# Optimization experiments

Hardware: AMD Instinct MI355X
Metric: run time of the kernel (lower is better)

## Reference

```python
import jax, jax.numpy as jnp
import numpy as np

D_MODEL = 1024
N_HEADS = 16
HEAD_DIM = D_MODEL // N_HEADS
B, T_Q, T_CACHE = 2, 2048, 2048


def setup_inputs() -> dict:
    key = jax.random.key(0)
    ks = jax.random.split(key, 12)
    s = 1.0 / np.sqrt(D_MODEL)
    return {
        "x": jax.random.normal(ks[0], (B, T_Q, D_MODEL), jnp.float32),
        "k_cache": jax.random.normal(ks[1], (B, N_HEADS, T_CACHE, HEAD_DIM), jnp.float32),
        "v_cache": jax.random.normal(ks[2], (B, N_HEADS, T_CACHE, HEAD_DIM), jnp.float32),
        "Wq": jax.random.normal(ks[3], (D_MODEL, D_MODEL), jnp.float32) * s,
        "bq": jax.random.normal(ks[4], (D_MODEL,), jnp.float32) * s,
        "Wk": jax.random.normal(ks[5], (D_MODEL, D_MODEL), jnp.float32) * s,
        "bk": jax.random.normal(ks[6], (D_MODEL,), jnp.float32) * s,
        "Wv": jax.random.normal(ks[7], (D_MODEL, D_MODEL), jnp.float32) * s,
        "bv": jax.random.normal(ks[8], (D_MODEL,), jnp.float32) * s,
        "Wo": jax.random.normal(ks[9], (D_MODEL, D_MODEL), jnp.float32) * s,
        "bo": jax.random.normal(ks[10], (D_MODEL,), jnp.float32) * s,
    }


def reference(x, k_cache, v_cache, Wq, bq, Wk, bk, Wv, bv, Wo, bo):
    B_, T, C = x.shape
    H, Dh = N_HEADS, HEAD_DIM
    scale = Dh ** -0.5

    def proj(W, b):
        # [B,T,C] -> [B,H,T,Dh]
        y = jnp.einsum('btc,cd->btd', x, W) + b
        return y.reshape(B_, T, H, Dh).transpose(0, 2, 1, 3)

    q = proj(Wq, bq)
    k = jnp.concatenate([k_cache, proj(Wk, bk)], axis=2)
    v = jnp.concatenate([v_cache, proj(Wv, bv)], axis=2)

    Tq, Tk = q.shape[2], k.shape[2]
    scores = jnp.einsum('bhqd,bhkd->bhqk', q, k) * scale  # [B,H,Tq,Tk]
    # causal: query i attends to keys j <= i + (Tk - Tq)
    i = jnp.arange(Tq)[:, None]
    j = jnp.arange(Tk)[None, :]
    mask = j > i + (Tk - Tq)
    scores = jnp.where(mask, -jnp.inf, scores)
    attn = jax.nn.softmax(scores, axis=-1)
    out = jnp.einsum('bhqk,bhkd->bhqd', attn, v)
    out = out.transpose(0, 2, 1, 3).reshape(B_, T, C)
    out = jnp.einsum('btc,cd->btd', out, Wo) + bo
    return out, (k, v)
```

## Files before the change

kernel.cpp:

```cpp
#include <hip/hip_runtime.h>
#include <hip/hip_bf16.h>
#include <cstdint>
#include <cstddef>

#define DM 1024
#define NH 16
#define DH 64
#define BB 2
#define TQ 2048
#define TCACHE 2048
#define TKTOT 4096
#define MROWS 4096

typedef __attribute__((ext_vector_type(8))) short bf16x8;
typedef __attribute__((ext_vector_type(4))) short bf16x4;
typedef __attribute__((ext_vector_type(4))) float f32x4;
typedef __attribute__((ext_vector_type(16))) float f32x16;

__device__ __forceinline__ unsigned pk2(float a, float b) {
  unsigned r;
  asm("v_cvt_pk_bf16_f32 %0, %1, %2" : "=v"(r) : "v"(a), "v"(b));
  return r;
}

__device__ __forceinline__ short f2bf(float f) {
  return (short)(unsigned short)pk2(f, f);
}

__device__ __forceinline__ uint2 pk4(float x, float y, float z, float w) {
  uint2 r;
  r.x = pk2(x, y);
  r.y = pk2(z, w);
  return r;
}

__device__ __forceinline__ float bf2f(short s) {
  union { unsigned u; float f; } v;
  v.u = ((unsigned)(unsigned short)s) << 16;
  return v.f;
}

__device__ __forceinline__ float exp2fast(float x) {
#if __has_builtin(__builtin_amdgcn_exp2f)
  return __builtin_amdgcn_exp2f(x);
#else
  return exp2f(x);
#endif
}

__device__ __forceinline__ void plswap(unsigned& a, unsigned& b) {
  asm volatile("v_permlane32_swap_b32 %0, %1" : "+v"(a), "+v"(b));
}

__device__ __forceinline__ void gld_lds16(const short* g, short* l) {
  __builtin_amdgcn_global_load_lds(
      (const __attribute__((address_space(1))) void*)((uintptr_t)g),
      (__attribute__((address_space(3))) void*)((uintptr_t)l), 16, 0, 0);
}

__global__ __launch_bounds__(256) void k_prep(
    const float* __restrict__ x, short* __restrict__ xb,
    const float* __restrict__ W0, const float* __restrict__ W1,
    const float* __restrict__ W2, const float* __restrict__ W3,
    short* __restrict__ Wt,
    const float* __restrict__ kc, short* __restrict__ Kb,
    const float* __restrict__ vc, short* __restrict__ Vtb) {
  __shared__ short lds[64 * 65];
  const int bid = (int)blockIdx.x;
  if (bid < 4096) {
    const size_t i = (size_t)bid * 256 + threadIdx.x;
    const float4 v = ((const float4*)x)[i];
    *(uint2*)(((short4*)xb) + i) = pk4(v.x, v.y, v.z, v.w);
  } else if (bid < 8192) {
    const int local = bid - 4096;
    const int bx = local & 31, by = (local >> 5) & 31, bz = local >> 10;
    short (*tile)[33] = (short(*)[33])lds;
    const float* W = (bz == 0) ? W0 : (bz == 1) ? W1 : (bz == 2) ? W2 : W3;
    short* dst = Wt + (size_t)bz * DM * DM;
    const int k0 = by * 32, n0 = bx * 32;
    const int tx = threadIdx.x & 31, ty = threadIdx.x >> 5;
#pragma unroll
    for (int r = 0; r < 4; r++) {
      const int k = ty + r * 8;
      tile[k][tx] = f2bf(W[(size_t)(k0 + k) * DM + n0 + tx]);
    }
    __syncthreads();
#pragma unroll
    for (int r = 0; r < 4; r++) {
      const int n = ty + r * 8;
      dst[(size_t)(n0 + n) * DM + k0 + tx] = tile[tx][n];
    }
  } else if (bid < 12288) {
    const size_t i = (size_t)(bid - 8192) * 256 + threadIdx.x;
    const float4 v = ((const float4*)kc)[i];
    const size_t e = i * 4;
    const int dh = (int)(e & 63);
    const int t = (int)((e >> 6) & 2047);
    const int bh = (int)(e >> 17);
    *(uint2*)(Kb + ((size_t)bh * TKTOT + t) * DH + dh) = pk4(v.x, v.y, v.z, v.w);
  } else {
    const int local = bid - 12288;
    const int bh = local >> 5;
    const int t0 = (local & 31) * 64;
    short (*tile)[65] = (short(*)[65])lds;
    const int tx = threadIdx.x & 15, ty = threadIdx.x >> 4;
    const float* src = vc + ((size_t)bh * TCACHE + t0) * DH;
#pragma unroll
    for (int r = 0; r < 4; r++) {
      const int t = ty + r * 16;
      const float4 v = *(const float4*)(src + (size_t)t * DH + tx * 4);
      tile[tx * 4 + 0][t] = f2bf(v.x);
      tile[tx * 4 + 1][t] = f2bf(v.y);
      tile[tx * 4 + 2][t] = f2bf(v.z);
      tile[tx * 4 + 3][t] = f2bf(v.w);
    }
    __syncthreads();
    short* vt = Vtb + (size_t)bh * DH * TKTOT + t0;
#pragma unroll
    for (int r = 0; r < 4; r++) {
      const int dh = ty + r * 16;
      short4 o;
      o.x = tile[dh][tx * 4 + 0];
      o.y = tile[dh][tx * 4 + 1];
      o.z = tile[dh][tx * 4 + 2];
      o.w = tile[dh][tx * 4 + 3];
      *(short4*)(vt + (size_t)dh * TKTOT + tx * 4) = o;
    }
  }
}

__global__ __launch_bounds__(256) void k_gemm(
    const short* __restrict__ A, const short* __restrict__ Bt,
    const float* __restrict__ b0, const float* __restrict__ b1, const float* __restrict__ b2,
    const int is_qkv, float* __restrict__ fdst,
    short* __restrict__ Qb, short* __restrict__ Kb, short* __restrict__ Vtb) {
  const int z = is_qkv ? (int)blockIdx.z : 3;
  const short* Bz = Bt + (is_qkv ? (size_t)z * DM * DM : 0);
  const float* bias = (z == 0 || z == 3) ? b0 : (z == 1 ? b1 : b2);

  __shared__ short sA[2][128 * 32];
  __shared__ short sB[2][128 * 32];

  const int m0 = blockIdx.y * 128;
  const int n0 = blockIdx.x * 128;
  const int tid = threadIdx.x;
  const int wv = tid >> 6;
  const int lane = tid & 63;
  const int quad = lane >> 4;
  const int l16 = lane & 15;
  const int wm = (wv >> 1) * 64;
  const int wn = (wv & 1) * 64;

  const f32x4 zero = {0.f, 0.f, 0.f, 0.f};
  f32x4 acc[4][4];
#pragma unroll
  for (int i = 0; i < 4; i++)
#pragma unroll
    for (int j = 0; j < 4; j++) acc[i][j] = zero;

  const int sw = (quad ^ ((l16 >> 1) & 3)) << 4;
  const int afo = (wm + l16) * 64 + sw;
  const int bfo = (wn + l16) * 64 + sw;

#define STAGEG(k0_, b_)                                                         \
  do {                                                                          \
    _Pragma("unroll") for (int s = 0; s < 2; s++) {                             \
      const int c = tid + s * 256;                                              \
      const int row = c >> 2, cs = c & 3;                                       \
      const int gc = cs ^ ((row >> 1) & 3);                                     \
      gld_lds16(A + (size_t)(m0 + row) * DM + (k0_) + gc * 8, &sA[b_][c * 8]);  \
      gld_lds16(Bz + (size_t)(n0 + row) * DM + (k0_) + gc * 8, &sB[b_][c * 8]); \
    }                                                                           \
  } while (0)

  STAGEG(0, 0);
  __syncthreads();
  int buf = 0;
  for (int k0 = 0; k0 < DM; k0 += 32) {
    if (k0 + 32 < DM) STAGEG(k0 + 32, buf ^ 1);
    const char* Ab = (const char*)&sA[0][0] + buf * 8192;
    const char* Bb = (const char*)&sB[0][0] + buf * 8192;
    bf16x8 af[4], bfv[4];
#pragma unroll
    for (int i = 0; i < 4; i++) af[i] = *(const bf16x8*)(Ab + afo + i * 1024);
#pragma unroll
    for (int j = 0; j < 4; j++) bfv[j] = *(const bf16x8*)(Bb + bfo + j * 1024);
    __builtin_amdgcn_s_setprio(1);
#pragma unroll
    for (int i = 0; i < 4; i++)
#pragma unroll
      for (int j = 0; j < 4; j++)
        acc[i][j] = __builtin_amdgcn_mfma_f32_16x16x32_bf16(af[i], bfv[j], acc[i][j], 0, 0, 0);
    __builtin_amdgcn_s_setprio(0);
    __syncthreads();
    buf ^= 1;
  }
#undef STAGEG

#pragma unroll
  for (int i = 0; i < 4; i++) {
#pragma unroll
    for (int j = 0; j < 4; j++) {
      const int gn = n0 + wn + j * 16 + l16;
      const float bb = bias[gn];
#pragma unroll
      for (int r = 0; r < 4; r++) {
        const int gm = m0 + wm + i * 16 + quad * 4 + r;
        const float v = acc[i][j][r] + bb;
        if (z == 3) {
          fdst[(size_t)gm * DM + gn] = v;
        } else {
          const int b_ = gm >> 11, t = gm & 2047;
          const int h_ = gn >> 6, dh = gn & 63;
          if (z == 0) {
            Qb[(((size_t)(b_ * NH + h_)) * TQ + t) * DH + dh] = f2bf(v * 0.18033688011f);
          } else if (z == 1) {
            Kb[(((size_t)(b_ * NH + h_)) * TKTOT + TCACHE + t) * DH + dh] = f2bf(v);
          } else {
            Vtb[(((size_t)(b_ * NH + h_)) * DH + dh) * TKTOT + TCACHE + t] = f2bf(v);
          }
        }
      }
    }
  }
}

__global__ __launch_bounds__(256, 4) void k_attn_expand(
    const short* __restrict__ Qb, const short* __restrict__ Kb,
    const short* __restrict__ Vtb, short* __restrict__ AOb,
    const float* __restrict__ kc, float* __restrict__ kF,
    const float* __restrict__ vc, float* __restrict__ vF) {
  __shared__ short SH[16384];

  const int bid = (int)blockIdx.x;
  if (bid < 512) {
    const int y = bid >> 5;
    const int bh = bid & 31;
    const int qx = (y < 8) ? (15 - y) : (y - 8);
    const int q0 = qx * 128;
    const int tid = threadIdx.x;
    const int wq = tid >> 6;
    const int lane = tid & 63;
    const int l32 = lane & 31;
    const int h = lane >> 5;

    const int nkt = 2 * qx + 34;

    const short* Kg = Kb + (size_t)bh * TKTOT * DH;
    const short* Vtg = Vtb + (size_t)bh * DH * TKTOT;

    const int c0 = tid, c1 = tid + 256;
    const int r0 = c0 >> 3, g0 = ((c0 & 7) ^ (r0 & 7)) * 8;
    const int r1 = c1 >> 3, g1 = ((c1 & 7) ^ (r1 & 7)) * 8;
    const short* Kst0 = Kg + (size_t)r0 * DH + g0;
    const short* Kst1 = Kg + (size_t)r1 * DH + g1;
    const short* Vst0 = Vtg + (size_t)r0 * TKTOT + g0;
    const short* Vst1 = Vtg + (size_t)r1 * TKTOT + g1;

    const short* Qrow = Qb + ((size_t)bh * TQ + q0 + wq * 32 + l32) * DH;
    bf16x8 qf[4];
#pragma unroll
    for (int s = 0; s < 4; s++) qf[s] = *(const bf16x8*)(Qrow + s * 16 + h * 8);

    const char* sKc = (const char*)SH;
    const char* sVc = (const char*)SH + 16384;
    const int rx7 = l32 & 7;
    const int base0 = l32 * 128;
    const int base1 = base0 + 4096;
    int co[4];
#pragma unroll
    for (int ks = 0; ks < 4; ks++) co[ks] = ((2 * ks + h) ^ rx7) << 4;

    const f32x16 zerov = {0, 0, 0, 0, 0, 0, 0, 0, 0, 0, 0, 0, 0, 0, 0, 0};
    f32x16 of0 = zerov;
    f32x16 of1 = zerov;
    float la = 0.f, lb = 0.f, lc = 0.f, ld = 0.f;

#define STAGE(t_, b_)                                    \
    do {                                                 \
      const size_t koff = (size_t)(t_) * 64 * DH;        \
      const size_t voff = (size_t)(t_) * 64;             \
      short* dK = SH + (b_)*4096;                        \
      short* dV = SH + 8192 + (b_)*4096;                 \
      gld_lds16(Kst0 + koff, dK + c0 * 8);               \
      gld_lds16(Kst1 + koff, dK + c1 * 8);               \
      gld_lds16(Vst0 + voff, dV + c0 * 8);               \
      gld_lds16(Vst1 + voff, dV + c1 * 8);               \
    } while (0)

    STAGE(0, 0);
    __syncthreads();
    int buf = 0;

    for (int t = 0; t < nkt; t++) {
      if (t + 1 < nkt) STAGE(t + 1, buf ^ 1);
      const char* kb_ = sKc + buf * 8192;
      const char* vb_ = sVc + buf * 8192;

      f32x16 sacc0, sacc1;
      __builtin_amdgcn_s_setprio(1);
      {
        const bf16x8 kf0 = *(const bf16x8*)(kb_ + base0 + co[0]);
        const bf16x8 kf1 = *(const bf16x8*)(kb_ + base1 + co[0]);
        sacc0 = __builtin_amdgcn_mfma_f32_32x32x16_bf16(kf0, qf[0], zerov, 0, 0, 0);
        sacc1 = __builtin_amdgcn_mfma_f32_32x32x16_bf16(kf1, qf[0], zerov, 0, 0, 0);
      }
#pragma unroll
      for (int ks = 1; ks < 4; ks++) {
        const bf16x8 kf0 = *(const bf16x8*)(kb_ + base0 + co[ks]);
        const bf16x8 kf1 = *(const bf16x8*)(kb_ + base1 + co[ks]);
        sacc0 = __builtin_amdgcn_mfma_f32_32x32x16_bf16(kf0, qf[ks], sacc0, 0, 0, 0);
        sacc1 = __builtin_amdgcn_mfma_f32_32x32x16_bf16(kf1, qf[ks], sacc1, 0, 0, 0);
      }
      __builtin_amdgcn_s_setprio(0);

      if (t >= nkt - 2) {
        const int qgl = q0 + wq * 32 + l32 + TCACHE;
        const int kb0 = t * 64 + 4 * h;
#pragma unroll
        for (int r = 0; r < 16; r++) {
          const int key = kb0 + (r & 3) + 8 * (r >> 2);
          if (key > qgl) sacc0[r] = -1e30f;
          if (key + 32 > qgl) sacc1[r] = -1e30f;
        }
      }
#pragma unroll
      for (int r = 0; r < 16; r++) {
        const float e0 = exp2fast(sacc0[r]);
        const float e1 = exp2fast(sacc1[r]);
        sacc0[r] = e0;
        sacc1[r] = e1;
        if ((r & 3) == 0) la += e0 + e1;
        else if ((r & 3) == 1) lb += e0 + e1;
        else if ((r & 3) == 2) lc += e0 + e1;
        else ld += e0 + e1;
      }

      bf16x8 pa[4];
#pragma unroll
      for (int s = 0; s < 4; s++) {
        const int o = (s & 1) * 8;
        unsigned w0, w1, w2, w3;
        if (s < 2) {
          w0 = pk2(sacc0[o + 0], sacc0[o + 1]);
          w1 = pk2(sacc0[o + 2], sacc0[o + 3]);
          w2 = pk2(sacc0[o + 4], sacc0[o + 5]);
          w3 = pk2(sacc0[o + 6], sacc0[o + 7]);
        } else {
          w0 = pk2(sacc1[o + 0], sacc1[o + 1]);
          w1 = pk2(sacc1[o + 2], sacc1[o + 3]);
          w2 = pk2(sacc1[o + 4], sacc1[o + 5]);
          w3 = pk2(sacc1[o + 6], sacc1[o + 7]);
        }
        plswap(w0, w2);
        plswap(w1, w3);
        union { unsigned u[4]; bf16x8 v; } pu;
        pu.u[0] = w0; pu.u[1] = w1; pu.u[2] = w2; pu.u[3] = w3;
        pa[s] = pu.v;
      }

      __builtin_amdgcn_s_setprio(1);
#pragma unroll
      for (int ks = 0; ks < 4; ks++) {
        const bf16x8 vf0 = *(const bf16x8*)(vb_ + base0 + co[ks]);
        const bf16x8 vf1 = *(const bf16x8*)(vb_ + base1 + co[ks]);
        of0 = __builtin_amdgcn_mfma_f32_32x32x16_bf16(pa[ks], vf0, of0, 0, 0, 0);
        of1 = __builtin_amdgcn_mfma_f32_32x32x16_bf16(pa[ks], vf1, of1, 0, 0, 0);
      }
      __builtin_amdgcn_s_setprio(0);
      __syncthreads();
      buf ^= 1;
    }
#undef STAGE

    float* sLf = (float*)SH;
    const float l_lane = (la + lb) + (lc + ld);
    const float l_tot = l_lane + __shfl_xor(l_lane, 32);
    if (h == 0) sLf[wq * 32 + l32] = l_tot;
    const int b_ = bh >> 4, h_ = bh & 15;
#pragma unroll
    for (int r = 0; r < 16; r++) {
      const int row = (r & 3) + 8 * (r >> 2) + 4 * h;
      const float inv = 1.f / sLf[wq * 32 + row];
      const int qg = q0 + wq * 32 + row;
      short* d = AOb + ((size_t)(b_ * TQ + qg)) * DM + h_ * 64;
      d[l32] = f2bf(of0[r] * inv);
      d[32 + l32] = f2bf(of1[r] * inv);
    }
  } else if (bid < 8704) {
    const size_t f4 = (size_t)(bid - 512) * 256 + threadIdx.x;
    const size_t e = f4 * 4;
    const int t = (int)((e >> 6) & 4095);
    float4 v;
    if (t < TCACHE) {
      const int dh = (int)(e & 63);
      const int bh = (int)(e >> 18);
      v = *(const float4*)(kc + ((size_t)(bh * TCACHE + t)) * DH + dh);
    } else {
      const short4 s = *(const short4*)(Kb + e);
      v.x = bf2f(s.x); v.y = bf2f(s.y); v.z = bf2f(s.z); v.w = bf2f(s.w);
    }
    *(float4*)(kF + e) = v;
  } else {
    const int local = bid - 8704;
    const int tt = local & 63, bh = local >> 6;
    short* tile = SH;
    if (tt < 32) {
#pragma unroll
      for (int k2 = 0; k2 < 4; k2++) {
        const int f = threadIdx.x + k2 * 256;
        const int trow = f >> 4, dh4 = f & 15;
        const size_t si = ((size_t)(bh * TCACHE) + tt * 64 + trow) * DH + dh4 * 4;
        const size_t di = ((size_t)(bh * TKTOT) + tt * 64 + trow) * DH + dh4 * 4;
        *(float4*)(vF + di) = *(const float4*)(vc + si);
      }
    } else {
      const int t0 = tt * 64;
#pragma unroll
      for (int k2 = 0; k2 < 4; k2++) {
        const int f = threadIdx.x + k2 * 256;
        const int dh = f >> 4, tc4 = f & 15;
        const short4 s = *(const short4*)(Vtb + ((size_t)(bh * DH + dh)) * TKTOT + t0 + tc4 * 4);
        *(short4*)(&tile[dh * 72 + tc4 * 4]) = s;
      }
      __syncthreads();
#pragma unroll
      for (int k2 = 0; k2 < 4; k2++) {
        const int f = threadIdx.x + k2 * 256;
        const int trow = f >> 4, dh4 = f & 15;
        float4 v;
        v.x = bf2f(tile[(dh4 * 4 + 0) * 72 + trow]);
        v.y = bf2f(tile[(dh4 * 4 + 1) * 72 + trow]);
        v.z = bf2f(tile[(dh4 * 4 + 2) * 72 + trow]);
        v.w = bf2f(tile[(dh4 * 4 + 3) * 72 + trow]);
        *(float4*)(vF + ((size_t)(bh * TKTOT) + t0 + trow) * DH + dh4 * 4) = v;
      }
    }
  }
}


extern "C" void kernel_launch(void* const* d_in, const int* in_sizes, int n_in,
                              void* d_out, int out_size, void* d_ws, size_t ws_size,
                              hipStream_t stream) {
  const float* x = (const float*)d_in[0];
  const float* kc = (const float*)d_in[1];
  const float* vc = (const float*)d_in[2];
  const float* Wq = (const float*)d_in[3];
  const float* bq = (const float*)d_in[4];
  const float* Wk = (const float*)d_in[5];
  const float* bk = (const float*)d_in[6];
  const float* Wv = (const float*)d_in[7];
  const float* bv = (const float*)d_in[8];
  const float* Wo = (const float*)d_in[9];
  const float* bo = (const float*)d_in[10];

  float* out = (float*)d_out;
  float* kF = out + (size_t)BB * TQ * DM;
  float* vF = kF + (size_t)BB * NH * TKTOT * DH;

  char* ws = (char*)d_ws;
  short* xb = (short*)ws;   ws += (size_t)MROWS * DM * 2;
  short* Wt = (short*)ws;   ws += (size_t)4 * DM * DM * 2;
  short* Qb = (short*)ws;   ws += (size_t)BB * NH * TQ * DH * 2;
  short* Kb = (short*)ws;   ws += (size_t)BB * NH * TKTOT * DH * 2;
  short* Vtb = (short*)ws;  ws += (size_t)BB * NH * TKTOT * DH * 2;
  short* AOb = (short*)ws;

  k_prep<<<13312, 256, 0, stream>>>(x, xb, Wq, Wk, Wv, Wo, Wt, kc, Kb, vc, Vtb);
  k_gemm<<<dim3(DM / 128, MROWS / 128, 3), 256, 0, stream>>>(
      xb, Wt, bq, bk, bv, 1, nullptr, Qb, Kb, Vtb);
  k_attn_expand<<<10752, 256, 0, stream>>>(Qb, Kb, Vtb, AOb, kc, kF, vc, vF);
  k_gemm<<<dim3(DM / 128, MROWS / 128, 1), 256, 0, stream>>>(
      AOb, Wt + (size_t)3 * DM * DM, bo, bo, bo, 0, out, nullptr, nullptr, nullptr);
}
```

Measured before the change: 271.0 us.

## Load attention K/V directly from global and overlap cache conversion with QKV GEMM

The attention loop no longer stages K and V tiles through double-buffered LDS with barriers. Each wave now loads its K/V fragments straight from global memory into registers, and the occupancy hint is lowered from 4 to 2. Separately, the K-cache bf16 conversion and V-cache transpose move from the prep kernel into the QKV GEMM launch as extra blocks, so they can run alongside the GEMM. This removes LDS traffic and syncs, but waves sharing a key tile now each fetch it from L2, and register pressure rises.

```diff
diff --git a/kernel.cpp b/kernel.cpp
--- a/kernel.cpp
+++ b/kernel.cpp
@@ -13,7 +13,6 @@
 #define MROWS 4096
 
 typedef __attribute__((ext_vector_type(8))) short bf16x8;
-typedef __attribute__((ext_vector_type(4))) short bf16x4;
 typedef __attribute__((ext_vector_type(4))) float f32x4;
 typedef __attribute__((ext_vector_type(16))) float f32x16;
 
@@ -62,16 +61,14 @@
     const float* __restrict__ x, short* __restrict__ xb,
     const float* __restrict__ W0, const float* __restrict__ W1,
     const float* __restrict__ W2, const float* __restrict__ W3,
-    short* __restrict__ Wt,
-    const float* __restrict__ kc, short* __restrict__ Kb,
-    const float* __restrict__ vc, short* __restrict__ Vtb) {
-  __shared__ short lds[64 * 65];
+    short* __restrict__ Wt) {
+  __shared__ short lds[32 * 33];
   const int bid = (int)blockIdx.x;
   if (bid < 4096) {
     const size_t i = (size_t)bid * 256 + threadIdx.x;
     const float4 v = ((const float4*)x)[i];
     *(uint2*)(((short4*)xb) + i) = pk4(v.x, v.y, v.z, v.w);
-  } else if (bid < 8192) {
+  } else {
     const int local = bid - 4096;
     const int bx = local & 31, by = (local >> 5) & 31, bz = local >> 10;
     short (*tile)[33] = (short(*)[33])lds;
@@ -90,126 +87,91 @@
       const int n = ty + r * 8;
       dst[(size_t)(n0 + n) * DM + k0 + tx] = tile[tx][n];
     }
-  } else if (bid < 12288) {
-    const size_t i = (size_t)(bid - 8192) * 256 + threadIdx.x;
-    const float4 v = ((const float4*)kc)[i];
-    const size_t e = i * 4;
-    const int dh = (int)(e & 63);
-    const int t = (int)((e >> 6) & 2047);
-    const int bh = (int)(e >> 17);
-    *(uint2*)(Kb + ((size_t)bh * TKTOT + t) * DH + dh) = pk4(v.x, v.y, v.z, v.w);
-  } else {
-    const int local = bid - 12288;
-    const int bh = local >> 5;
-    const int t0 = (local & 31) * 64;
-    short (*tile)[65] = (short(*)[65])lds;
-    const int tx = threadIdx.x & 15, ty = threadIdx.x >> 4;
-    const float* src = vc + ((size_t)bh * TCACHE + t0) * DH;
-#pragma unroll
-    for (int r = 0; r < 4; r++) {
-      const int t = ty + r * 16;
-      const float4 v = *(const float4*)(src + (size_t)t * DH + tx * 4);
-      tile[tx * 4 + 0][t] = f2bf(v.x);
-      tile[tx * 4 + 1][t] = f2bf(v.y);
-      tile[tx * 4 + 2][t] = f2bf(v.z);
-      tile[tx * 4 + 3][t] = f2bf(v.w);
-    }
-    __syncthreads();
-    short* vt = Vtb + (size_t)bh * DH * TKTOT + t0;
-#pragma unroll
-    for (int r = 0; r < 4; r++) {
-      const int dh = ty + r * 16;
-      short4 o;
-      o.x = tile[dh][tx * 4 + 0];
-      o.y = tile[dh][tx * 4 + 1];
-      o.z = tile[dh][tx * 4 + 2];
-      o.w = tile[dh][tx * 4 + 3];
-      *(short4*)(vt + (size_t)dh * TKTOT + tx * 4) = o;
-    }
   }
 }
 
-__global__ __launch_bounds__(256) void k_gemm(
+__global__ __launch_bounds__(256) void k_qkv(
     const short* __restrict__ A, const short* __restrict__ Bt,
     const float* __restrict__ b0, const float* __restrict__ b1, const float* __restrict__ b2,
-    const int is_qkv, float* __restrict__ fdst,
-    short* __restrict__ Qb, short* __restrict__ Kb, short* __restrict__ Vtb) {
-  const int z = is_qkv ? (int)blockIdx.z : 3;
-  const short* Bz = Bt + (is_qkv ? (size_t)z * DM * DM : 0);
-  const float* bias = (z == 0 || z == 3) ? b0 : (z == 1 ? b1 : b2);
-
-  __shared__ short sA[2][128 * 32];
-  __shared__ short sB[2][128 * 32];
-
-  const int m0 = blockIdx.y * 128;
-  const int n0 = blockIdx.x * 128;
-  const int tid = threadIdx.x;
-  const int wv = tid >> 6;
-  const int lane = tid & 63;
-  const int quad = lane >> 4;
-  const int l16 = lane & 15;
-  const int wm = (wv >> 1) * 64;
-  const int wn = (wv & 1) * 64;
-
-  const f32x4 zero = {0.f, 0.f, 0.f, 0.f};
-  f32x4 acc[4][4];
-#pragma unroll
-  for (int i = 0; i < 4; i++)
-#pragma unroll
-    for (int j = 0; j < 4; j++) acc[i][j] = zero;
-
-  const int sw = (quad ^ ((l16 >> 1) & 3)) << 4;
-  const int afo = (wm + l16) * 64 + sw;
-  const int bfo = (wn + l16) * 64 + sw;
-
-#define STAGEG(k0_, b_)                                                         \
-  do {                                                                          \
-    _Pragma("unroll") for (int s = 0; s < 2; s++) {                             \
-      const int c = tid + s * 256;                                              \
-      const int row = c >> 2, cs = c & 3;                                       \
-      const int gc = cs ^ ((row >> 1) & 3);                                     \
-      gld_lds16(A + (size_t)(m0 + row) * DM + (k0_) + gc * 8, &sA[b_][c * 8]);  \
-      gld_lds16(Bz + (size_t)(n0 + row) * DM + (k0_) + gc * 8, &sB[b_][c * 8]); \
-    }                                                                           \
-  } while (0)
-
-  STAGEG(0, 0);
-  __syncthreads();
-  int buf = 0;
-  for (int k0 = 0; k0 < DM; k0 += 32) {
-    if (k0 + 32 < DM) STAGEG(k0 + 32, buf ^ 1);
-    const char* Ab = (const char*)&sA[0][0] + buf * 8192;
-    const char* Bb = (const char*)&sB[0][0] + buf * 8192;
-    bf16x8 af[4], bfv[4];
-#pragma unroll
-    for (int i = 0; i < 4; i++) af[i] = *(const bf16x8*)(Ab + afo + i * 1024);
-#pragma unroll
-    for (int j = 0; j < 4; j++) bfv[j] = *(const bf16x8*)(Bb + bfo + j * 1024);
-    __builtin_amdgcn_s_setprio(1);
+    short* __restrict__ Qb, short* __restrict__ Kb, short* __restrict__ Vtb,
+    const float* __restrict__ kc, const float* __restrict__ vc) {
+  __shared__ short SH[16384];
+  const int bid = (int)blockIdx.x;
+  if (bid < 768) {
+    const int z = bid >> 8;
+    const int by = (bid >> 3) & 31;
+    const int bx = bid & 7;
+    const short* Bz = Bt + (size_t)z * DM * DM;
+    const float* bias = (z == 0) ? b0 : (z == 1 ? b1 : b2);
+
+    const int m0 = by * 128;
+    const int n0 = bx * 128;
+    const int tid = threadIdx.x;
+    const int wv = tid >> 6;
+    const int lane = tid & 63;
+    const int quad = lane >> 4;
+    const int l16 = lane & 15;
+    const int wm = (wv >> 1) * 64;
+    const int wn = (wv & 1) * 64;
+
+    const f32x4 zero = {0.f, 0.f, 0.f, 0.f};
+    f32x4 acc[4][4];
 #pragma unroll
     for (int i = 0; i < 4; i++)
 #pragma unroll
-      for (int j = 0; j < 4; j++)
-        acc[i][j] = __builtin_amdgcn_mfma_f32_16x16x32_bf16(af[i], bfv[j], acc[i][j], 0, 0, 0);
-    __builtin_amdgcn_s_setprio(0);
+      for (int j = 0; j < 4; j++) acc[i][j] = zero;
+
+    const int sw = (quad ^ ((l16 >> 1) & 3)) << 4;
+    const int afo = (wm + l16) * 64 + sw;
+    const int bfo = (wn + l16) * 64 + sw;
+
+#define STAGEG(k0_, b_)                                                              \
+    do {                                                                             \
+      _Pragma("unroll") for (int s = 0; s < 2; s++) {                                \
+        const int c = tid + s * 256;                                                 \
+        const int row = c >> 2, cs = c & 3;                                          \
+        const int gc = cs ^ ((row >> 1) & 3);                                        \
+        gld_lds16(A + (size_t)(m0 + row) * DM + (k0_) + gc * 8,                      \
+                  SH + (b_) * 4096 + c * 8);                                         \
+        gld_lds16(Bz + (size_t)(n0 + row) * DM + (k0_) + gc * 8,                     \
+                  SH + 8192 + (b_) * 4096 + c * 8);                                  \
+      }                                                                              \
+    } while (0)
+
+    STAGEG(0, 0);
     __syncthreads();
-    buf ^= 1;
-  }
+    int buf = 0;
+    for (int k0 = 0; k0 < DM; k0 += 32) {
+      if (k0 + 32 < DM) STAGEG(k0 + 32, buf ^ 1);
+      const char* Ab = (const char*)SH + buf * 8192;
+      const char* Bb = (const char*)SH + 16384 + buf * 8192;
+      bf16x8 af[4], bfv[4];
+#pragma unroll
+      for (int i = 0; i < 4; i++) af[i] = *(const bf16x8*)(Ab + afo + i * 1024);
+#pragma unroll
+      for (int j = 0; j < 4; j++) bfv[j] = *(const bf16x8*)(Bb + bfo + j * 1024);
+      __builtin_amdgcn_s_setprio(1);
+#pragma unroll
+      for (int i = 0; i < 4; i++)
+#pragma unroll
+        for (int j = 0; j < 4; j++)
+          acc[i][j] = __builtin_amdgcn_mfma_f32_16x16x32_bf16(af[i], bfv[j], acc[i][j], 0, 0, 0);
+      __builtin_amdgcn_s_setprio(0);
+      __syncthreads();
+      buf ^= 1;
+    }
 #undef STAGEG
 
 #pragma unroll
-  for (int i = 0; i < 4; i++) {
-#pragma unroll
-    for (int j = 0; j < 4; j++) {
-      const int gn = n0 + wn + j * 16 + l16;
-      const float bb = bias[gn];
-#pragma unroll
-      for (int r = 0; r < 4; r++) {
-        const int gm = m0 + wm + i * 16 + quad * 4 + r;
-        const float v = acc[i][j][r] + bb;
-        if (z == 3) {
-          fdst[(size_t)gm * DM + gn] = v;
-        } else {
+    for (int i = 0; i < 4; i++) {
+#pragma unroll
+      for (int j = 0; j < 4; j++) {
+        const int gn = n0 + wn + j * 16 + l16;
+        const float bb = bias[gn];
+#pragma unroll
+        for (int r = 0; r < 4; r++) {
+          const int gm = m0 + wm + i * 16 + quad * 4 + r;
+          const float v = acc[i][j][r] + bb;
           const int b_ = gm >> 11, t = gm & 2047;
           const int h_ = gn >> 6, dh = gn & 63;
           if (z == 0) {
@@ -222,15 +184,128 @@
         }
       }
     }
+  } else if (bid < 4864) {
+    const size_t i = (size_t)(bid - 768) * 256 + threadIdx.x;
+    const float4 v = ((const float4*)kc)[i];
+    const size_t e = i * 4;
+    const int dh = (int)(e & 63);
+    const int t = (int)((e >> 6) & 2047);
+    const int bh = (int)(e >> 17);
+    *(uint2*)(Kb + ((size_t)bh * TKTOT + t) * DH + dh) = pk4(v.x, v.y, v.z, v.w);
+  } else {
+    const int local = bid - 4864;
+    const int bh = local >> 5;
+    const int t0 = (local & 31) * 64;
+    short (*tile)[65] = (short(*)[65])SH;
+    const int tx = threadIdx.x & 15, ty = threadIdx.x >> 4;
+    const float* src = vc + ((size_t)bh * TCACHE + t0) * DH;
+#pragma unroll
+    for (int r = 0; r < 4; r++) {
+      const int t = ty + r * 16;
+      const float4 v = *(const float4*)(src + (size_t)t * DH + tx * 4);
+      tile[tx * 4 + 0][t] = f2bf(v.x);
+      tile[tx * 4 + 1][t] = f2bf(v.y);
+      tile[tx * 4 + 2][t] = f2bf(v.z);
+      tile[tx * 4 + 3][t] = f2bf(v.w);
+    }
+    __syncthreads();
+    short* vt = Vtb + (size_t)bh * DH * TKTOT + t0;
+#pragma unroll
+    for (int r = 0; r < 4; r++) {
+      const int dh = ty + r * 16;
+      short4 o;
+      o.x = tile[dh][tx * 4 + 0];
+      o.y = tile[dh][tx * 4 + 1];
+      o.z = tile[dh][tx * 4 + 2];
+      o.w = tile[dh][tx * 4 + 3];
+      *(short4*)(vt + (size_t)dh * TKTOT + tx * 4) = o;
+    }
   }
 }
 
-__global__ __launch_bounds__(256, 4) void k_attn_expand(
+__global__ __launch_bounds__(256) void k_gemm(
+    const short* __restrict__ A, const short* __restrict__ Bt,
+    const float* __restrict__ bias, float* __restrict__ fdst) {
+  __shared__ short sA[2][128 * 32];
+  __shared__ short sB[2][128 * 32];
+
+  const int m0 = blockIdx.y * 128;
+  const int n0 = blockIdx.x * 128;
+  const int tid = threadIdx.x;
+  const int wv = tid >> 6;
+  const int lane = tid & 63;
+  const int quad = lane >> 4;
+  const int l16 = lane & 15;
+  const int wm = (wv >> 1) * 64;
+  const int wn = (wv & 1) * 64;
+
+  const f32x4 zero = {0.f, 0.f, 0.f, 0.f};
+  f32x4 acc[4][4];
+#pragma unroll
+  for (int i = 0; i < 4; i++)
+#pragma unroll
+    for (int j = 0; j < 4; j++) acc[i][j] = zero;
+
+  const int sw = (quad ^ ((l16 >> 1) & 3)) << 4;
+  const int afo = (wm + l16) * 64 + sw;
+  const int bfo = (wn + l16) * 64 + sw;
+
+#define STAGEG(k0_, b_)                                                         \
+  do {                                                                          \
+    _Pragma("unroll") for (int s = 0; s < 2; s++) {                             \
+      const int c = tid + s * 256;                                              \
+      const int row = c >> 2, cs = c & 3;                                       \
+      const int gc = cs ^ ((row >> 1) & 3);                                     \
+      gld_lds16(A + (size_t)(m0 + row) * DM + (k0_) + gc * 8, &sA[b_][c * 8]);  \
+      gld_lds16(Bt + (size_t)(n0 + row) * DM + (k0_) + gc * 8, &sB[b_][c * 8]); \
+    }                                                                           \
+  } while (0)
+
+  STAGEG(0, 0);
+  __syncthreads();
+  int buf = 0;
+  for (int k0 = 0; k0 < DM; k0 += 32) {
+    if (k0 + 32 < DM) STAGEG(k0 + 32, buf ^ 1);
+    const char* Ab = (const char*)&sA[0][0] + buf * 8192;
+    const char* Bb = (const char*)&sB[0][0] + buf * 8192;
+    bf16x8 af[4], bfv[4];
+#pragma unroll
+    for (int i = 0; i < 4; i++) af[i] = *(const bf16x8*)(Ab + afo + i * 1024);
+#pragma unroll
+    for (int j = 0; j < 4; j++) bfv[j] = *(const bf16x8*)(Bb + bfo + j * 1024);
+    __builtin_amdgcn_s_setprio(1);
+#pragma unroll
+    for (int i = 0; i < 4; i++)
+#pragma unroll
+      for (int j = 0; j < 4; j++)
+        acc[i][j] = __builtin_amdgcn_mfma_f32_16x16x32_bf16(af[i], bfv[j], acc[i][j], 0, 0, 0);
+    __builtin_amdgcn_s_setprio(0);
+    __syncthreads();
+    buf ^= 1;
+  }
+#undef STAGEG
+
+#pragma unroll
+  for (int i = 0; i < 4; i++) {
+#pragma unroll
+    for (int j = 0; j < 4; j++) {
+      const int gn = n0 + wn + j * 16 + l16;
+      const float bb = bias[gn];
+#pragma unroll
+      for (int r = 0; r < 4; r++) {
+        const int gm = m0 + wm + i * 16 + quad * 4 + r;
+        fdst[(size_t)gm * DM + gn] = acc[i][j][r] + bb;
+      }
+    }
+  }
+}
+
+__global__ __launch_bounds__(256, 2) void k_attn_expand(
     const short* __restrict__ Qb, const short* __restrict__ Kb,
     const short* __restrict__ Vtb, short* __restrict__ AOb,
     const float* __restrict__ kc, float* __restrict__ kF,
     const float* __restrict__ vc, float* __restrict__ vF) {
-  __shared__ short SH[16384];
+  __shared__ short SH[64 * 72];
 
   const int bid = (int)blockIdx.x;
   if (bid < 512) {
@@ -249,70 +324,49 @@
     const short* Kg = Kb + (size_t)bh * TKTOT * DH;
     const short* Vtg = Vtb + (size_t)bh * DH * TKTOT;
 
-    const int c0 = tid, c1 = tid + 256;
-    const int r0 = c0 >> 3, g0 = ((c0 & 7) ^ (r0 & 7)) * 8;
-    const int r1 = c1 >> 3, g1 = ((c1 & 7) ^ (r1 & 7)) * 8;
-    const short* Kst0 = Kg + (size_t)r0 * DH + g0;
-    const short* Kst1 = Kg + (size_t)r1 * DH + g1;
-    const short* Vst0 = Vtg + (size_t)r0 * TKTOT + g0;
-    const short* Vst1 = Vtg + (size_t)r1 * TKTOT + g1;
+    const short* kr0 = Kg + (size_t)l32 * DH + 8 * h;
+    const short* kr1 = Kg + (size_t)(l32 + 32) * DH + 8 * h;
+    const short* vr0 = Vtg + (size_t)l32 * TKTOT + 8 * h;
+    const short* vr1 = Vtg + (size_t)(l32 + 32) * TKTOT + 8 * h;
 
     const short* Qrow = Qb + ((size_t)bh * TQ + q0 + wq * 32 + l32) * DH;
     bf16x8 qf[4];
 #pragma unroll
     for (int s = 0; s < 4; s++) qf[s] = *(const bf16x8*)(Qrow + s * 16 + h * 8);
-
-    const char* sKc = (const char*)SH;
-    const char* sVc = (const char*)SH + 16384;
-    const int rx7 = l32 & 7;
-    const int base0 = l32 * 128;
-    const int base1 = base0 + 4096;
-    int co[4];
-#pragma unroll
-    for (int ks = 0; ks < 4; ks++) co[ks] = ((2 * ks + h) ^ rx7) << 4;
 
     const f32x16 zerov = {0, 0, 0, 0, 0, 0, 0, 0, 0, 0, 0, 0, 0, 0, 0, 0};
     f32x16 of0 = zerov;
     f32x16 of1 = zerov;
     float la = 0.f, lb = 0.f, lc = 0.f, ld = 0.f;
 
-#define STAGE(t_, b_)                                    \
-    do {                                                 \
-      const size_t koff = (size_t)(t_) * 64 * DH;        \
-      const size_t voff = (size_t)(t_) * 64;             \
-      short* dK = SH + (b_)*4096;                        \
-      short* dV = SH + 8192 + (b_)*4096;                 \
-      gld_lds16(Kst0 + koff, dK + c0 * 8);               \
-      gld_lds16(Kst1 + koff, dK + c1 * 8);               \
-      gld_lds16(Vst0 + voff, dV + c0 * 8);               \
-      gld_lds16(Vst1 + voff, dV + c1 * 8);               \
-    } while (0)
-
-    STAGE(0, 0);
-    __syncthreads();
-    int buf = 0;
-
     for (int t = 0; t < nkt; t++) {
-      if (t + 1 < nkt) STAGE(t + 1, buf ^ 1);
-      const char* kb_ = sKc + buf * 8192;
-      const char* vb_ = sVc + buf * 8192;
+      const size_t kbase = (size_t)t * (64 * DH);
+      const size_t vbase = (size_t)t * 64;
+
+      bf16x8 kf0[4], kf1[4];
+#pragma unroll
+      for (int ks = 0; ks < 4; ks++) {
+        kf0[ks] = *(const bf16x8*)(kr0 + kbase + ks * 16);
+        kf1[ks] = *(const bf16x8*)(kr1 + kbase + ks * 16);
+      }
 
       f32x16 sacc0, sacc1;
       __builtin_amdgcn_s_setprio(1);
-      {
-        const bf16x8 kf0 = *(const bf16x8*)(kb_ + base0 + co[0]);
-        const bf16x8 kf1 = *(const bf16x8*)(kb_ + base1 + co[0]);
-        sacc0 = __builtin_amdgcn_mfma_f32_32x32x16_bf16(kf0, qf[0], zerov, 0, 0, 0);
-        sacc1 = __builtin_amdgcn_mfma_f32_32x32x16_bf16(kf1, qf[0], zerov, 0, 0, 0);
-      }
+      sacc0 = __builtin_amdgcn_mfma_f32_32x32x16_bf16(kf0[0], qf[0], zerov, 0, 0, 0);
+      sacc1 = __builtin_amdgcn_mfma_f32_32x32x16_bf16(kf1[0], qf[0], zerov, 0, 0, 0);
 #pragma unroll
       for (int ks = 1; ks < 4; ks++) {
-        const bf16x8 kf0 = *(const bf16x8*)(kb_ + base0 + co[ks]);
-        const bf16x8 kf1 = *(const bf16x8*)(kb_ + base1 + co[ks]);
-        sacc0 = __builtin_amdgcn_mfma_f32_32x32x16_bf16(kf0, qf[ks], sacc0, 0, 0, 0);
-        sacc1 = __builtin_amdgcn_mfma_f32_32x32x16_bf16(kf1, qf[ks], sacc1, 0, 0, 0);
+        sacc0 = __builtin_amdgcn_mfma_f32_32x32x16_bf16(kf0[ks], qf[ks], sacc0, 0, 0, 0);
+        sacc1 = __builtin_amdgcn_mfma_f32_32x32x16_bf16(kf1[ks], qf[ks], sacc1, 0, 0, 0);
       }
       __builtin_amdgcn_s_setprio(0);
+
+      bf16x8 vf0[4], vf1[4];
+#pragma unroll
+      for (int ks = 0; ks < 4; ks++) {
+        vf0[ks] = *(const bf16x8*)(vr0 + vbase + ks * 16);
+        vf1[ks] = *(const bf16x8*)(vr1 + vbase + ks * 16);
+      }
 
       if (t >= nkt - 2) {
         const int qgl = q0 + wq * 32 + l32 + TCACHE;
@@ -362,16 +416,11 @@
       __builtin_amdgcn_s_setprio(1);
 #pragma unroll
       for (int ks = 0; ks < 4; ks++) {
-        const bf16x8 vf0 = *(const bf16x8*)(vb_ + base0 + co[ks]);
-        const bf16x8 vf1 = *(const bf16x8*)(vb_ + base1 + co[ks]);
-        of0 = __builtin_amdgcn_mfma_f32_32x32x16_bf16(pa[ks], vf0, of0, 0, 0, 0);
-        of1 = __builtin_amdgcn_mfma_f32_32x32x16_bf16(pa[ks], vf1, of1, 0, 0, 0);
+        of0 = __builtin_amdgcn_mfma_f32_32x32x16_bf16(pa[ks], vf0[ks], of0, 0, 0, 0);
+        of1 = __builtin_amdgcn_mfma_f32_32x32x16_bf16(pa[ks], vf1[ks], of1, 0, 0, 0);
       }
       __builtin_amdgcn_s_setprio(0);
-      __syncthreads();
-      buf ^= 1;
-    }
-#undef STAGE
+    }
 
     float* sLf = (float*)SH;
     const float l_lane = (la + lb) + (lc + ld);
@@ -467,10 +516,8 @@
   short* Vtb = (short*)ws;  ws += (size_t)BB * NH * TKTOT * DH * 2;
   short* AOb = (short*)ws;
 
-  k_prep<<<13312, 256, 0, stream>>>(x, xb, Wq, Wk, Wv, Wo, Wt, kc, Kb, vc, Vtb);
-  k_gemm<<<dim3(DM / 128, MROWS / 128, 3), 256, 0, stream>>>(
-      xb, Wt, bq, bk, bv, 1, nullptr, Qb, Kb, Vtb);
+  k_prep<<<8192, 256, 0, stream>>>(x, xb, Wq, Wk, Wv, Wo, Wt);
+  k_qkv<<<5888, 256, 0, stream>>>(xb, Wt, bq, bk, bv, Qb, Kb, Vtb, kc, vc);
   k_attn_expand<<<10752, 256, 0, stream>>>(Qb, Kb, Vtb, AOb, kc, kF, vc, vF);
-  k_gemm<<<dim3(DM / 128, MROWS / 128, 1), 256, 0, stream>>>(
-      AOb, Wt + (size_t)3 * DM * DM, bo, bo, bo, 0, out, nullptr, nullptr, nullptr);
-}
+  k_gemm<<<dim3(8, 32), 256, 0, stream>>>(AOb, Wt + (size_t)3 * DM * DM, bo, out);
+}
```

Result: slower. 386.6 us (+42.7%).
